# Kernel optimization log

Measured on AMD Instinct MI355X. Metric: run time of the kernel, lower is better.

Reference implementation:

```python
import jax, jax.numpy as jnp
import numpy as np

B, N, DS, DP, H, DH = 2, 512, 384, 128, 16, 64
MAX_SEQ = 2048
DI = H * DH  # inner attention dim = 1024
LN_EPS = 1e-5


def setup_inputs() -> dict:
    key = jax.random.key(0)
    ks = jax.random.split(key, 10)
    s = 0.02  # param init scale
    return {
        "single_repr": jax.random.normal(ks[0], (B, N, DS), jnp.float32),
        "pairwise_repr": jax.random.normal(ks[1], (B, N, N, DP), jnp.float32),
        "ln_gamma": jnp.ones((DP,), jnp.float32),
        "ln_beta": jnp.zeros((DP,), jnp.float32),
        "w_bias": jax.random.normal(ks[2], (DP, H), jnp.float32) * s,
        "attn_bias_bias": jax.random.normal(ks[3], (MAX_SEQ, MAX_SEQ), jnp.float32) * s,
        "w_q": jax.random.normal(ks[4], (DS, DI), jnp.float32) * s,
        "w_k": jax.random.normal(ks[5], (DS, DI), jnp.float32) * s,
        "w_v": jax.random.normal(ks[6], (DS, DI), jnp.float32) * s,
        "w_g": jax.random.normal(ks[7], (DS, DI), jnp.float32) * s,
        "w_o": jax.random.normal(ks[8], (DI, DS), jnp.float32) * s,
    }


def reference(single_repr, pairwise_repr, ln_gamma, ln_beta, w_bias,
              attn_bias_bias, w_q, w_k, w_v, w_g, w_o):
    b, n, _ = single_repr.shape
    # LayerNorm over pairwise feature dim, then project to per-head bias
    mu = pairwise_repr.mean(-1, keepdims=True)
    var = pairwise_repr.var(-1, keepdims=True)
    pr = (pairwise_repr - mu) * jax.lax.rsqrt(var + LN_EPS) * ln_gamma + ln_beta
    # ... i j h -> ... h i j, plus learned positional bias slice
    attn_bias = jnp.einsum('bijd,dh->bhij', pr, w_bias) + attn_bias_bias[:n, :n]

    # multi-head attention with additive per-head bias and sigmoid gating
    q = (single_repr @ w_q).reshape(b, n, H, DH).transpose(0, 2, 1, 3)  # bhnd
    k = (single_repr @ w_k).reshape(b, n, H, DH).transpose(0, 2, 1, 3)
    v = (single_repr @ w_v).reshape(b, n, H, DH).transpose(0, 2, 1, 3)
    scale = DH ** -0.5
    scores = jnp.einsum('bhid,bhjd->bhij', q, k) * scale + attn_bias
    attn = jax.nn.softmax(scores, axis=-1)
    o = jnp.einsum('bhij,bhjd->bhid', attn, v)
    o = o.transpose(0, 2, 1, 3).reshape(b, n, DI)
    gates = jax.nn.sigmoid(single_repr @ w_g)
    return (o * gates) @ w_o
```

## Files before the change

kernel.cpp:

```cpp
#include <hip/hip_runtime.h>
#include <hip/hip_bf16.h>

#define B_ 2
#define N_ 512
#define DS_ 384
#define DP_ 128
#define H_ 16
#define DH_ 64
#define DI_ 1024
#define MAXSEQ 2048
#define PAD 8

typedef float f32x4 __attribute__((ext_vector_type(4)));
typedef short bf16x8 __attribute__((ext_vector_type(8)));

__device__ __forceinline__ unsigned short f2b(float f) {
    unsigned int u = __builtin_bit_cast(unsigned int, f);
    u += 0x7FFFu + ((u >> 16) & 1u);
    return (unsigned short)(u >> 16);
}
__device__ __forceinline__ float b2f(unsigned short s) {
    unsigned int u = ((unsigned int)s) << 16;
    return __builtin_bit_cast(float, u);
}

__global__ __launch_bounds__(256) void k_transpose_all(const float* __restrict__ wq,
                                                       const float* __restrict__ wk,
                                                       const float* __restrict__ wv,
                                                       const float* __restrict__ wg,
                                                       const float* __restrict__ wo,
                                                       const float* __restrict__ gamma,
                                                       const float* __restrict__ beta,
                                                       const float* __restrict__ wb,
                                                       unsigned short* __restrict__ Wt,
                                                       unsigned short* __restrict__ Wot,
                                                       unsigned short* __restrict__ GhG,
                                                       float* __restrict__ SsG,
                                                       float* __restrict__ TsG) {
    int z = blockIdx.z;
    if (z == 5) {
        if (blockIdx.x || blockIdx.y) return;
        int t = threadIdx.x;
        for (int idx = t; idx < DP_ * H_; idx += 256) {
            int d = idx >> 4, h = idx & 15;
            GhG[h * DP_ + d] = f2b(gamma[d] * wb[idx]);
        }
        if (t < 32) {
            int h = t & 15;
            const float* src = (t >= 16) ? beta : gamma;
            float s = 0.f;
            for (int d = 0; d < DP_; ++d) s = fmaf(src[d], wb[d * H_ + h], s);
            if (t >= 16) TsG[h] = s; else SsG[h] = s;
        }
        return;
    }
    __shared__ float tile[32][33];
    const float* in;
    unsigned short* out;
    int R, C;
    if (z < 4) {
        in = (z == 0) ? wq : (z == 1) ? wk : (z == 2) ? wv : wg;
        out = Wt + (long)z * 1024 * 384;
        R = 384; C = 1024;
    } else {
        in = wo; out = Wot; R = 1024; C = 384;
    }
    int c0 = blockIdx.x * 32, r0 = blockIdx.y * 32;
    if (c0 >= C || r0 >= R) return;
    int tx = threadIdx.x & 31, ty = threadIdx.x >> 5;
    #pragma unroll
    for (int i = ty; i < 32; i += 8)
        tile[i][tx] = in[(long)(r0 + i) * C + (c0 + tx)];
    __syncthreads();
    #pragma unroll
    for (int i = ty; i < 32; i += 8)
        out[(long)(c0 + i) * R + (r0 + tx)] = f2b(tile[tx][i]);
}

__global__ __launch_bounds__(256) void k_bias(const float* __restrict__ pw,
                                              const float* __restrict__ abb,
                                              const unsigned short* __restrict__ GhG,
                                              const float* __restrict__ SsG,
                                              const float* __restrict__ TsG,
                                              unsigned short* __restrict__ biasP) {
    __shared__ float Xs[64 * 128];
    __shared__ float rsum[4][16] __attribute__((aligned(16)));
    __shared__ float rsq[4][16] __attribute__((aligned(16)));
    int t = threadIdx.x;
    int w = t >> 6, lane = t & 63;
    int lane15 = lane & 15, kg = lane >> 4;
    long p0 = (long)blockIdx.x * 64;
    int i_blk = (int)((p0 >> 9) & (N_ - 1));
    int j0 = (int)(p0 & (N_ - 1));
    long bb = p0 >> 18;

    const char* src = (const char*)(pw + (p0 << 7));
    char* lds = (char*)Xs;
    #pragma unroll
    for (int c = 0; c < 8; ++c) {
        int L = c * 4096 + t * 16;
        int row = L >> 9, b = L & 511;
        uint4 v = *(const uint4*)(src + L);
        *(uint4*)(lds + (row << 9) + (b ^ ((row & 7) << 4))) = v;
    }

    bf16x8 gb[4];
    #pragma unroll
    for (int kk = 0; kk < 4; ++kk)
        gb[kk] = *(const bf16x8*)&GhG[lane15 * DP_ + kk * 32 + kg * 8];
    float sh = SsG[lane15], th = TsG[lane15];
    __syncthreads();

    int row = w * 16 + lane15;
    const char* rbase = lds + (row << 9);
    int sw = (lane15 & 7) << 4;
    f32x4 xa[4], xb4[4];
    #pragma unroll
    for (int kk = 0; kk < 4; ++kk) {
        int b0 = kk * 128 + kg * 32;
        xa[kk]  = *(const f32x4*)(rbase + ((b0) ^ sw));
        xb4[kk] = *(const f32x4*)(rbase + ((b0 + 16) ^ sw));
    }
    float s = 0.f, q = 0.f;
    #pragma unroll
    for (int kk = 0; kk < 4; ++kk) {
        s += xa[kk][0] + xa[kk][1] + xa[kk][2] + xa[kk][3];
        s += xb4[kk][0] + xb4[kk][1] + xb4[kk][2] + xb4[kk][3];
        #pragma unroll
        for (int e = 0; e < 4; ++e) {
            q = fmaf(xa[kk][e], xa[kk][e], q);
            q = fmaf(xb4[kk][e], xb4[kk][e], q);
        }
    }
    s += __shfl_xor(s, 16); s += __shfl_xor(s, 32);
    q += __shfl_xor(q, 16); q += __shfl_xor(q, 32);
    if (lane < 16) { rsum[w][lane15] = s; rsq[w][lane15] = q; }

    f32x4 acc = {};
    #pragma unroll
    for (int kk = 0; kk < 4; ++kk) {
        bf16x8 a;
        unsigned short* ap = (unsigned short*)&a;
        ap[0] = f2b(xa[kk][0]);  ap[1] = f2b(xa[kk][1]);
        ap[2] = f2b(xa[kk][2]);  ap[3] = f2b(xa[kk][3]);
        ap[4] = f2b(xb4[kk][0]); ap[5] = f2b(xb4[kk][1]);
        ap[6] = f2b(xb4[kk][2]); ap[7] = f2b(xb4[kk][3]);
        acc = __builtin_amdgcn_mfma_f32_16x16x32_bf16(a, gb[kk], acc, 0, 0, 0);
    }
    int jr = w * 16 + kg * 4;
    float4 rs = *(const float4*)&rsum[w][kg * 4];
    float4 rq = *(const float4*)&rsq[w][kg * 4];
    float4 av = *(const float4*)(abb + (long)i_blk * MAXSEQ + j0 + jr);
    unsigned short* planeBase = biasP + ((bb * H_ + lane15) * N_ + i_blk) * N_ + j0;
    ushort4 res;
    float mu, var;
    mu = rs.x * (1.f / DP_); var = fmaf(rq.x, 1.f / DP_, -mu * mu);
    res.x = f2b(fmaf(rsqrtf(var + 1e-5f), acc[0] - mu * sh, th + av.x));
    mu = rs.y * (1.f / DP_); var = fmaf(rq.y, 1.f / DP_, -mu * mu);
    res.y = f2b(fmaf(rsqrtf(var + 1e-5f), acc[1] - mu * sh, th + av.y));
    mu = rs.z * (1.f / DP_); var = fmaf(rq.z, 1.f / DP_, -mu * mu);
    res.z = f2b(fmaf(rsqrtf(var + 1e-5f), acc[2] - mu * sh, th + av.z));
    mu = rs.w * (1.f / DP_); var = fmaf(rq.w, 1.f / DP_, -mu * mu);
    res.w = f2b(fmaf(rsqrtf(var + 1e-5f), acc[3] - mu * sh, th + av.w));
    *(ushort4*)(planeBase + jr) = res;
}

__global__ __launch_bounds__(256) void k_proj(const float* __restrict__ X,
                                              const unsigned short* __restrict__ Wt,
                                              unsigned short* __restrict__ Qb,
                                              unsigned short* __restrict__ Kb,
                                              unsigned short* __restrict__ Vt,
                                              unsigned short* __restrict__ Xg) {
    __shared__ unsigned short As[128][64 + PAD];
    __shared__ unsigned short Bs[128][64 + PAD];
    int m0 = blockIdx.x * 128;
    int n0 = blockIdx.y * 128;
    int t = threadIdx.x;
    int wave = t >> 6, lane = t & 63;
    int wr = wave >> 1, wc = wave & 1;
    int lane15 = lane & 15, kg = lane >> 4;
    f32x4 acc[4][4] = {};
    for (int k0 = 0; k0 < DS_; k0 += 64) {
        __syncthreads();
        {
            int r = t >> 1, half = t & 1;
            const float4* src = (const float4*)(X + (long)(m0 + r) * DS_ + k0 + half * 32);
            unsigned short* dst = &As[r][half * 32];
            #pragma unroll
            for (int ii = 0; ii < 8; ++ii) {
                float4 v = src[ii];
                dst[ii * 4 + 0] = f2b(v.x); dst[ii * 4 + 1] = f2b(v.y);
                dst[ii * 4 + 2] = f2b(v.z); dst[ii * 4 + 3] = f2b(v.w);
            }
            const uint4* wsrc = (const uint4*)(Wt + (long)(n0 + r) * DS_ + k0 + half * 32);
            uint4* wdst = (uint4*)&Bs[r][half * 32];
            wdst[0] = wsrc[0]; wdst[1] = wsrc[1]; wdst[2] = wsrc[2]; wdst[3] = wsrc[3];
        }
        __syncthreads();
        #pragma unroll
        for (int ks = 0; ks < 2; ++ks) {
            bf16x8 a[4], bb[4];
            #pragma unroll
            for (int mf = 0; mf < 4; ++mf)
                a[mf] = *(const bf16x8*)&As[wr * 64 + mf * 16 + lane15][ks * 32 + kg * 8];
            #pragma unroll
            for (int nf = 0; nf < 4; ++nf)
                bb[nf] = *(const bf16x8*)&Bs[wc * 64 + nf * 16 + lane15][ks * 32 + kg * 8];
            #pragma unroll
            for (int mf = 0; mf < 4; ++mf)
                #pragma unroll
                for (int nf = 0; nf < 4; ++nf)
                    acc[mf][nf] = __builtin_amdgcn_mfma_f32_16x16x32_bf16(a[mf], bb[nf], acc[mf][nf], 0, 0, 0);
        }
    }
    int p = n0 >> 10;
    int lgrp = lane >> 4;
    #pragma unroll
    for (int mf = 0; mf < 4; ++mf) {
        #pragma unroll
        for (int nf = 0; nf < 4; ++nf) {
            int col = n0 + wc * 64 + nf * 16 + lane15;
            int ch = col & 1023;
            int h = ch >> 6, dh = ch & 63;
            int row0 = m0 + wr * 64 + mf * 16 + lgrp * 4;
            if (p == 0 || p == 1) {
                unsigned short* base = (p == 0) ? Qb : Kb;
                float scl = (p == 0) ? 0.125f : 1.0f;
                #pragma unroll
                for (int rr = 0; rr < 4; ++rr) {
                    int rowx = row0 + rr;
                    int b = rowx >> 9, n = rowx & 511;
                    base[(((long)(b * 16 + h)) * 512 + n) * 64 + dh] = f2b(acc[mf][nf][rr] * scl);
                }
            } else if (p == 2) {
                int b = row0 >> 9, n = row0 & 511;
                ushort4 v;
                v.x = f2b(acc[mf][nf][0]); v.y = f2b(acc[mf][nf][1]);
                v.z = f2b(acc[mf][nf][2]); v.w = f2b(acc[mf][nf][3]);
                *(ushort4*)&Vt[(((long)(b * 16 + h)) * 64 + dh) * 512 + n] = v;
            } else {
                #pragma unroll
                for (int rr = 0; rr < 4; ++rr) {
                    int rowx = row0 + rr;
                    Xg[(long)rowx * 1024 + ch] = f2b(acc[mf][nf][rr]);
                }
            }
        }
    }
}

__global__ __launch_bounds__(512) void k_flash(const unsigned short* __restrict__ Qb,
                                               const unsigned short* __restrict__ Kb,
                                               const unsigned short* __restrict__ Vt,
                                               const unsigned short* __restrict__ biasP,
                                               const unsigned short* __restrict__ Xg,
                                               unsigned short* __restrict__ Og) {
    __shared__ unsigned short Kt[2][64][72];
    __shared__ unsigned short Vs[2][64][72];
    __shared__ unsigned short Bt[2][64][72];
    __shared__ unsigned short Ps[8][16][72];
    __shared__ float Mscr[4][16], Lscr[4][16];
    __shared__ float Oscr[4][16][64];
    int bh = blockIdx.y;
    int b = bh >> 4, h = bh & 15;
    int i0 = blockIdx.x * 64;
    int t = threadIdx.x, w = t >> 6, lane = t & 63;
    int g = w & 3, jg = w >> 2;
    int lane15 = lane & 15, lgrp = lane >> 4;
    int tl = t & 255;
    int rs_ = tl >> 3, cs_ = tl & 7;

    bf16x8 qf[2];
    #pragma unroll
    for (int kk = 0; kk < 2; ++kk)
        qf[kk] = *(const bf16x8*)&Qb[((long)bh * 512 + i0 + g * 16 + lane15) * 64 + kk * 32 + lgrp * 8];

    float m_run = -1e30f, l_run = 0.f;
    f32x4 o[4] = {};

    for (int jtl = 0; jtl < 4; ++jtl) {
        int j0 = (jg * 4 + jtl) * 64;
        __syncthreads();
        {
            *(uint4*)&Kt[jg][rs_][cs_ * 8] = *(const uint4*)&Kb[((long)bh * 512 + j0 + rs_) * 64 + cs_ * 8];
            *(uint4*)&Vs[jg][rs_][cs_ * 8] = *(const uint4*)&Vt[((long)bh * 64 + rs_) * 512 + j0 + cs_ * 8];
            *(uint4*)&Bt[jg][rs_][cs_ * 8] = *(const uint4*)&biasP[((long)bh * 512 + i0 + rs_) * 512 + j0 + cs_ * 8];
            int r2 = rs_ + 32;
            *(uint4*)&Kt[jg][r2][cs_ * 8] = *(const uint4*)&Kb[((long)bh * 512 + j0 + r2) * 64 + cs_ * 8];
            *(uint4*)&Vs[jg][r2][cs_ * 8] = *(const uint4*)&Vt[((long)bh * 64 + r2) * 512 + j0 + cs_ * 8];
            *(uint4*)&Bt[jg][r2][cs_ * 8] = *(const uint4*)&biasP[((long)bh * 512 + i0 + r2) * 512 + j0 + cs_ * 8];
        }
        __syncthreads();

        f32x4 s[4];
        #pragma unroll
        for (int nf = 0; nf < 4; ++nf) {
            f32x4 z = {};
            #pragma unroll
            for (int kk = 0; kk < 2; ++kk) {
                bf16x8 af = *(const bf16x8*)&Kt[jg][nf * 16 + lane15][kk * 32 + lgrp * 8];
                z = __builtin_amdgcn_mfma_f32_16x16x32_bf16(af, qf[kk], z, 0, 0, 0);
            }
            s[nf] = z;
        }
        #pragma unroll
        for (int nf = 0; nf < 4; ++nf) {
            ushort4 bv = *(const ushort4*)&Bt[jg][g * 16 + lane15][nf * 16 + lgrp * 4];
            s[nf][0] += b2f(bv.x); s[nf][1] += b2f(bv.y);
            s[nf][2] += b2f(bv.z); s[nf][3] += b2f(bv.w);
        }

        float pmax = s[0][0];
        #pragma unroll
        for (int nf = 0; nf < 4; ++nf)
            #pragma unroll
            for (int rr = 0; rr < 4; ++rr) pmax = fmaxf(pmax, s[nf][rr]);
        pmax = fmaxf(pmax, __shfl_xor(pmax, 16));
        pmax = fmaxf(pmax, __shfl_xor(pmax, 32));
        float m_new = fmaxf(m_run, pmax);
        float scale = __expf(m_run - m_new);
        float psum = 0.f;
        #pragma unroll
        for (int nf = 0; nf < 4; ++nf)
            #pragma unroll
            for (int rr = 0; rr < 4; ++rr) {
                s[nf][rr] = __expf(s[nf][rr] - m_new);
                psum += s[nf][rr];
            }
        psum += __shfl_xor(psum, 16);
        psum += __shfl_xor(psum, 32);
        l_run = l_run * scale + psum;
        m_run = m_new;
        #pragma unroll
        for (int rr = 0; rr < 4; ++rr) {
            float sc = __shfl(scale, lgrp * 4 + rr);
            #pragma unroll
            for (int nf = 0; nf < 4; ++nf) o[nf][rr] *= sc;
        }
        #pragma unroll
        for (int nf = 0; nf < 4; ++nf) {
            ushort4 pv_;
            pv_.x = f2b(s[nf][0]); pv_.y = f2b(s[nf][1]);
            pv_.z = f2b(s[nf][2]); pv_.w = f2b(s[nf][3]);
            *(ushort4*)&Ps[w][lane15][nf * 16 + lgrp * 4] = pv_;
        }
        #pragma unroll
        for (int kk = 0; kk < 2; ++kk) {
            bf16x8 pa = *(const bf16x8*)&Ps[w][lane15][kk * 32 + lgrp * 8];
            #pragma unroll
            for (int nf = 0; nf < 4; ++nf) {
                bf16x8 vb = *(const bf16x8*)&Vs[jg][nf * 16 + lane15][kk * 32 + lgrp * 8];
                o[nf] = __builtin_amdgcn_mfma_f32_16x16x32_bf16(pa, vb, o[nf], 0, 0, 0);
            }
        }
    }

    __syncthreads();
    if (jg == 1) {
        if (lane < 16) { Mscr[g][lane] = m_run; Lscr[g][lane] = l_run; }
        #pragma unroll
        for (int nf = 0; nf < 4; ++nf)
            #pragma unroll
            for (int rr = 0; rr < 4; ++rr)
                Oscr[g][lgrp * 4 + rr][nf * 16 + lane15] = o[nf][rr];
    }
    __syncthreads();
    if (jg == 0) {
        #pragma unroll
        for (int rr = 0; rr < 4; ++rr) {
            int row = lgrp * 4 + rr;
            float m1 = __shfl(m_run, row);
            float l1 = __shfl(l_run, row);
            float m2 = Mscr[g][row];
            float l2 = Lscr[g][row];
            float mm = fmaxf(m1, m2);
            float e1 = __expf(m1 - mm), e2 = __expf(m2 - mm);
            float inv = 1.f / (l1 * e1 + l2 * e2);
            long grow = (long)b * 512 + i0 + g * 16 + row;
            #pragma unroll
            for (int nf = 0; nf < 4; ++nf) {
                int dh = nf * 16 + lane15;
                float o2 = Oscr[g][row][dh];
                float val = (o[nf][rr] * e1 + o2 * e2) * inv;
                float xgv = b2f(Xg[grow * 1024 + h * 64 + dh]);
                float gate = 1.f / (1.f + __expf(-xgv));
                Og[grow * 1024 + h * 64 + dh] = f2b(val * gate);
            }
        }
    }
}

__global__ __launch_bounds__(256) void k_out(const unsigned short* __restrict__ Og,
                                             const unsigned short* __restrict__ Wot,
                                             float* __restrict__ out) {
    __shared__ unsigned short As[64][64 + PAD];
    __shared__ unsigned short Bs[64][64 + PAD];
    int m0 = blockIdx.x * 64, n0 = blockIdx.y * 64;
    int t = threadIdx.x, wave = t >> 6, lane = t & 63;
    int wr = wave >> 1, wc = wave & 1;
    int lane15 = lane & 15, kg = lane >> 4;
    f32x4 acc[2][2] = {};
    for (int k0 = 0; k0 < 1024; k0 += 64) {
        __syncthreads();
        {
            int r = t >> 2, qd = t & 3;
            const uint4* s1 = (const uint4*)(Og + (long)(m0 + r) * 1024 + k0 + qd * 16);
            uint4* d1 = (uint4*)&As[r][qd * 16];
            d1[0] = s1[0]; d1[1] = s1[1];
            const uint4* s2 = (const uint4*)(Wot + (long)(n0 + r) * 1024 + k0 + qd * 16);
            uint4* d2 = (uint4*)&Bs[r][qd * 16];
            d2[0] = s2[0]; d2[1] = s2[1];
        }
        __syncthreads();
        #pragma unroll
        for (int ks = 0; ks < 2; ++ks) {
            bf16x8 a[2], bb[2];
            #pragma unroll
            for (int mf = 0; mf < 2; ++mf)
                a[mf] = *(const bf16x8*)&As[wr * 32 + mf * 16 + lane15][ks * 32 + kg * 8];
            #pragma unroll
            for (int nf = 0; nf < 2; ++nf)
                bb[nf] = *(const bf16x8*)&Bs[wc * 32 + nf * 16 + lane15][ks * 32 + kg * 8];
            #pragma unroll
            for (int mf = 0; mf < 2; ++mf)
                #pragma unroll
                for (int nf = 0; nf < 2; ++nf)
                    acc[mf][nf] = __builtin_amdgcn_mfma_f32_16x16x32_bf16(a[mf], bb[nf], acc[mf][nf], 0, 0, 0);
        }
    }
    int lgrp = lane >> 4;
    #pragma unroll
    for (int mf = 0; mf < 2; ++mf) {
        #pragma unroll
        for (int nf = 0; nf < 2; ++nf) {
            int col = n0 + wc * 32 + nf * 16 + lane15;
            int row0 = m0 + wr * 32 + mf * 16 + lgrp * 4;
            #pragma unroll
            for (int rr = 0; rr < 4; ++rr)
                out[(long)(row0 + rr) * DS_ + col] = acc[mf][nf][rr];
        }
    }
}

extern "C" void kernel_launch(void* const* d_in, const int* in_sizes, int n_in,
                              void* d_out, int out_size, void* d_ws, size_t ws_size,
                              hipStream_t stream) {
    const float* single = (const float*)d_in[0];
    const float* pw     = (const float*)d_in[1];
    const float* gamma  = (const float*)d_in[2];
    const float* beta   = (const float*)d_in[3];
    const float* wb     = (const float*)d_in[4];
    const float* abb    = (const float*)d_in[5];
    const float* wq     = (const float*)d_in[6];
    const float* wk     = (const float*)d_in[7];
    const float* wv     = (const float*)d_in[8];
    const float* wg     = (const float*)d_in[9];
    const float* wo     = (const float*)d_in[10];
    float* out = (float*)d_out;
    char* ws = (char*)d_ws;

    unsigned short* SP  = (unsigned short*)(ws);
    unsigned short* Qb  = (unsigned short*)(ws + 16777216);
    unsigned short* Kb  = (unsigned short*)(ws + 18874368);
    unsigned short* Vt  = (unsigned short*)(ws + 20971520);
    unsigned short* Xg  = (unsigned short*)(ws + 23068672);
    unsigned short* Og  = (unsigned short*)(ws + 25165824);
    unsigned short* Wt  = (unsigned short*)(ws + 27262976);
    unsigned short* Wot = (unsigned short*)(ws + 30408704);
    unsigned short* GhG = (unsigned short*)(ws + 31195136);
    float* SsG          = (float*)(ws + 31199232);
    float* TsG          = (float*)(ws + 31199296);

    k_transpose_all<<<dim3(32, 32, 6), 256, 0, stream>>>(wq, wk, wv, wg, wo,
                                                         gamma, beta, wb,
                                                         Wt, Wot, GhG, SsG, TsG);
    k_bias<<<8192, 256, 0, stream>>>(pw, abb, GhG, SsG, TsG, SP);
    k_proj<<<dim3(8, 32), 256, 0, stream>>>(single, Wt, Qb, Kb, Vt, Xg);
    k_flash<<<dim3(8, 32), 512, 0, stream>>>(Qb, Kb, Vt, SP, Xg, Og);
    k_out<<<dim3(16, 6), 256, 0, stream>>>(Og, Wot, out);
}
```

Before: 120.8 us.

## Fuse weight transpose into bias kernel, shrink proj tiles, swizzle flash LDS

Merges the weight-transpose/bf16-convert kernel into the LayerNorm bias kernel as extra blocks. Each bias block now recomputes the gamma*w_bias fragments and the per-head sums itself, which removes a launch and the dependency on a tiny single-block prologue. The projection GEMM M-tile drops from 128 to 64 rows, doubling its grid for better occupancy. The flash kernel replaces padded LDS tiles with XOR-swizzled ones and aliases the P and O scratch buffers to cut LDS use. In exchange, the transpose blocks get scheduled alongside the heavy bias blocks, and every bias block does redundant small global loads.

Result: no change. 121.5 us (+0.6%).

```diff
diff --git a/kernel.cpp b/kernel.cpp
--- a/kernel.cpp
+++ b/kernel.cpp
@@ -24,72 +24,55 @@
     return __builtin_bit_cast(float, u);
 }
 
-__global__ __launch_bounds__(256) void k_transpose_all(const float* __restrict__ wq,
-                                                       const float* __restrict__ wk,
-                                                       const float* __restrict__ wv,
-                                                       const float* __restrict__ wg,
-                                                       const float* __restrict__ wo,
-                                                       const float* __restrict__ gamma,
-                                                       const float* __restrict__ beta,
-                                                       const float* __restrict__ wb,
-                                                       unsigned short* __restrict__ Wt,
-                                                       unsigned short* __restrict__ Wot,
-                                                       unsigned short* __restrict__ GhG,
-                                                       float* __restrict__ SsG,
-                                                       float* __restrict__ TsG) {
-    int z = blockIdx.z;
-    if (z == 5) {
-        if (blockIdx.x || blockIdx.y) return;
-        int t = threadIdx.x;
-        for (int idx = t; idx < DP_ * H_; idx += 256) {
-            int d = idx >> 4, h = idx & 15;
-            GhG[h * DP_ + d] = f2b(gamma[d] * wb[idx]);
-        }
-        if (t < 32) {
-            int h = t & 15;
-            const float* src = (t >= 16) ? beta : gamma;
-            float s = 0.f;
-            for (int d = 0; d < DP_; ++d) s = fmaf(src[d], wb[d * H_ + h], s);
-            if (t >= 16) TsG[h] = s; else SsG[h] = s;
-        }
-        return;
-    }
-    __shared__ float tile[32][33];
-    const float* in;
-    unsigned short* out;
-    int R, C;
-    if (z < 4) {
-        in = (z == 0) ? wq : (z == 1) ? wk : (z == 2) ? wv : wg;
-        out = Wt + (long)z * 1024 * 384;
-        R = 384; C = 1024;
-    } else {
-        in = wo; out = Wot; R = 1024; C = 384;
-    }
-    int c0 = blockIdx.x * 32, r0 = blockIdx.y * 32;
-    if (c0 >= C || r0 >= R) return;
-    int tx = threadIdx.x & 31, ty = threadIdx.x >> 5;
-    #pragma unroll
-    for (int i = ty; i < 32; i += 8)
-        tile[i][tx] = in[(long)(r0 + i) * C + (c0 + tx)];
-    __syncthreads();
-    #pragma unroll
-    for (int i = ty; i < 32; i += 8)
-        out[(long)(c0 + i) * R + (r0 + tx)] = f2b(tile[tx][i]);
-}
-
-__global__ __launch_bounds__(256) void k_bias(const float* __restrict__ pw,
-                                              const float* __restrict__ abb,
-                                              const unsigned short* __restrict__ GhG,
-                                              const float* __restrict__ SsG,
-                                              const float* __restrict__ TsG,
-                                              unsigned short* __restrict__ biasP) {
+#define SW(row, bc) ((bc) ^ (((row) & 7) << 4))
+
+__global__ __launch_bounds__(256) void k_pre(const float* __restrict__ pw,
+                                             const float* __restrict__ abb,
+                                             const float* __restrict__ gamma,
+                                             const float* __restrict__ beta,
+                                             const float* __restrict__ wb,
+                                             const float* __restrict__ wq,
+                                             const float* __restrict__ wk,
+                                             const float* __restrict__ wv,
+                                             const float* __restrict__ wg,
+                                             const float* __restrict__ wo,
+                                             unsigned short* __restrict__ Wt,
+                                             unsigned short* __restrict__ Wot,
+                                             unsigned short* __restrict__ biasP) {
     __shared__ float Xs[64 * 128];
     __shared__ float rsum[4][16] __attribute__((aligned(16)));
     __shared__ float rsq[4][16] __attribute__((aligned(16)));
+    int bid = blockIdx.x;
     int t = threadIdx.x;
+
+    if (bid >= 8192) {
+        int tid = bid - 8192;
+        int z = tid / 384, r = tid % 384;
+        const float* in; unsigned short* out; int C, Rr, c0, r0;
+        if (z < 4) {
+            in = (z == 0) ? wq : (z == 1) ? wk : (z == 2) ? wv : wg;
+            out = Wt + (long)z * 1024 * 384;
+            C = 1024; Rr = 384;
+            c0 = (r & 31) * 32; r0 = (r >> 5) * 32;
+        } else {
+            in = wo; out = Wot; C = 384; Rr = 1024;
+            c0 = (r % 12) * 32; r0 = (r / 12) * 32;
+        }
+        float (*tile)[33] = (float(*)[33])Xs;
+        int tx = t & 31, ty = t >> 5;
+        #pragma unroll
+        for (int i = ty; i < 32; i += 8)
+            tile[i][tx] = in[(long)(r0 + i) * C + (c0 + tx)];
+        __syncthreads();
+        #pragma unroll
+        for (int i = ty; i < 32; i += 8)
+            out[(long)(c0 + i) * Rr + (r0 + tx)] = f2b(tile[tx][i]);
+        return;
+    }
+
     int w = t >> 6, lane = t & 63;
     int lane15 = lane & 15, kg = lane >> 4;
-    long p0 = (long)blockIdx.x * 64;
+    long p0 = (long)bid * 64;
     int i_blk = (int)((p0 >> 9) & (N_ - 1));
     int j0 = (int)(p0 & (N_ - 1));
     long bb = p0 >> 18;
@@ -104,11 +87,26 @@
         *(uint4*)(lds + (row << 9) + (b ^ ((row & 7) << 4))) = v;
     }
 
+    float shp = 0.f, thp = 0.f;
     bf16x8 gb[4];
     #pragma unroll
-    for (int kk = 0; kk < 4; ++kk)
-        gb[kk] = *(const bf16x8*)&GhG[lane15 * DP_ + kk * 32 + kg * 8];
-    float sh = SsG[lane15], th = TsG[lane15];
+    for (int kk = 0; kk < 4; ++kk) {
+        bf16x8 a;
+        unsigned short* ap = (unsigned short*)&a;
+        #pragma unroll
+        for (int e = 0; e < 8; ++e) {
+            int d = kk * 32 + kg * 8 + e;
+            float wv_ = wb[d * 16 + lane15];
+            float gv = gamma[d];
+            ap[e] = f2b(gv * wv_);
+            shp = fmaf(gv, wv_, shp);
+            thp = fmaf(beta[d], wv_, thp);
+        }
+        gb[kk] = a;
+    }
+    shp += __shfl_xor(shp, 16); shp += __shfl_xor(shp, 32);
+    thp += __shfl_xor(thp, 16); thp += __shfl_xor(thp, 32);
+    float sh = shp, th = thp;
     __syncthreads();
 
     int row = w * 16 + lane15;
@@ -171,58 +169,59 @@
                                               unsigned short* __restrict__ Kb,
                                               unsigned short* __restrict__ Vt,
                                               unsigned short* __restrict__ Xg) {
-    __shared__ unsigned short As[128][64 + PAD];
+    __shared__ unsigned short As[64][64 + PAD];
     __shared__ unsigned short Bs[128][64 + PAD];
-    int m0 = blockIdx.x * 128;
+    int m0 = blockIdx.x * 64;
     int n0 = blockIdx.y * 128;
     int t = threadIdx.x;
     int wave = t >> 6, lane = t & 63;
     int wr = wave >> 1, wc = wave & 1;
     int lane15 = lane & 15, kg = lane >> 4;
-    f32x4 acc[4][4] = {};
+    int rA = t >> 2, qA = t & 3;
+    int rB = t >> 1, hB = t & 1;
+    f32x4 acc[2][4] = {};
     for (int k0 = 0; k0 < DS_; k0 += 64) {
         __syncthreads();
         {
-            int r = t >> 1, half = t & 1;
-            const float4* src = (const float4*)(X + (long)(m0 + r) * DS_ + k0 + half * 32);
-            unsigned short* dst = &As[r][half * 32];
-            #pragma unroll
-            for (int ii = 0; ii < 8; ++ii) {
-                float4 v = src[ii];
-                dst[ii * 4 + 0] = f2b(v.x); dst[ii * 4 + 1] = f2b(v.y);
-                dst[ii * 4 + 2] = f2b(v.z); dst[ii * 4 + 3] = f2b(v.w);
-            }
-            const uint4* wsrc = (const uint4*)(Wt + (long)(n0 + r) * DS_ + k0 + half * 32);
-            uint4* wdst = (uint4*)&Bs[r][half * 32];
-            wdst[0] = wsrc[0]; wdst[1] = wsrc[1]; wdst[2] = wsrc[2]; wdst[3] = wsrc[3];
+            const float4* srcA = (const float4*)(X + (long)(m0 + rA) * DS_ + k0 + qA * 16);
+            unsigned short* dstA = &As[rA][qA * 16];
+            #pragma unroll
+            for (int ii = 0; ii < 4; ++ii) {
+                float4 v = srcA[ii];
+                dstA[ii * 4 + 0] = f2b(v.x); dstA[ii * 4 + 1] = f2b(v.y);
+                dstA[ii * 4 + 2] = f2b(v.z); dstA[ii * 4 + 3] = f2b(v.w);
+            }
+            const uint4* srcB = (const uint4*)(Wt + (long)(n0 + rB) * DS_ + k0 + hB * 32);
+            uint4* dstB = (uint4*)&Bs[rB][hB * 32];
+            dstB[0] = srcB[0]; dstB[1] = srcB[1]; dstB[2] = srcB[2]; dstB[3] = srcB[3];
         }
         __syncthreads();
         #pragma unroll
         for (int ks = 0; ks < 2; ++ks) {
-            bf16x8 a[4], bb[4];
-            #pragma unroll
-            for (int mf = 0; mf < 4; ++mf)
-                a[mf] = *(const bf16x8*)&As[wr * 64 + mf * 16 + lane15][ks * 32 + kg * 8];
+            bf16x8 a[2], bbv[4];
+            #pragma unroll
+            for (int mf = 0; mf < 2; ++mf)
+                a[mf] = *(const bf16x8*)&As[wr * 32 + mf * 16 + lane15][ks * 32 + kg * 8];
             #pragma unroll
             for (int nf = 0; nf < 4; ++nf)
-                bb[nf] = *(const bf16x8*)&Bs[wc * 64 + nf * 16 + lane15][ks * 32 + kg * 8];
-            #pragma unroll
-            for (int mf = 0; mf < 4; ++mf)
+                bbv[nf] = *(const bf16x8*)&Bs[wc * 64 + nf * 16 + lane15][ks * 32 + kg * 8];
+            #pragma unroll
+            for (int mf = 0; mf < 2; ++mf)
                 #pragma unroll
                 for (int nf = 0; nf < 4; ++nf)
-                    acc[mf][nf] = __builtin_amdgcn_mfma_f32_16x16x32_bf16(a[mf], bb[nf], acc[mf][nf], 0, 0, 0);
+                    acc[mf][nf] = __builtin_amdgcn_mfma_f32_16x16x32_bf16(a[mf], bbv[nf], acc[mf][nf], 0, 0, 0);
         }
     }
     int p = n0 >> 10;
     int lgrp = lane >> 4;
     #pragma unroll
-    for (int mf = 0; mf < 4; ++mf) {
+    for (int mf = 0; mf < 2; ++mf) {
         #pragma unroll
         for (int nf = 0; nf < 4; ++nf) {
             int col = n0 + wc * 64 + nf * 16 + lane15;
             int ch = col & 1023;
             int h = ch >> 6, dh = ch & 63;
-            int row0 = m0 + wr * 64 + mf * 16 + lgrp * 4;
+            int row0 = m0 + wr * 32 + mf * 16 + lgrp * 4;
             if (p == 0 || p == 1) {
                 unsigned short* base = (p == 0) ? Qb : Kb;
                 float scl = (p == 0) ? 0.125f : 1.0f;
@@ -255,12 +254,13 @@
                                                const unsigned short* __restrict__ biasP,
                                                const unsigned short* __restrict__ Xg,
                                                unsigned short* __restrict__ Og) {
-    __shared__ unsigned short Kt[2][64][72];
-    __shared__ unsigned short Vs[2][64][72];
-    __shared__ unsigned short Bt[2][64][72];
-    __shared__ unsigned short Ps[8][16][72];
+    __shared__ unsigned short Kt[2][64][64];
+    __shared__ unsigned short Vs[2][64][64];
+    __shared__ unsigned short Bt[2][64][64];
+    __shared__ char PsOscr[16384];
     __shared__ float Mscr[4][16], Lscr[4][16];
-    __shared__ float Oscr[4][16][64];
+    unsigned short (*Ps)[16][64] = (unsigned short(*)[16][64])PsOscr;
+    float (*Oscr)[16][64] = (float(*)[16][64])PsOscr;
     int bh = blockIdx.y;
     int b = bh >> 4, h = bh & 15;
     int i0 = blockIdx.x * 64;
@@ -282,13 +282,19 @@
         int j0 = (jg * 4 + jtl) * 64;
         __syncthreads();
         {
-            *(uint4*)&Kt[jg][rs_][cs_ * 8] = *(const uint4*)&Kb[((long)bh * 512 + j0 + rs_) * 64 + cs_ * 8];
-            *(uint4*)&Vs[jg][rs_][cs_ * 8] = *(const uint4*)&Vt[((long)bh * 64 + rs_) * 512 + j0 + cs_ * 8];
-            *(uint4*)&Bt[jg][rs_][cs_ * 8] = *(const uint4*)&biasP[((long)bh * 512 + i0 + rs_) * 512 + j0 + cs_ * 8];
             int r2 = rs_ + 32;
-            *(uint4*)&Kt[jg][r2][cs_ * 8] = *(const uint4*)&Kb[((long)bh * 512 + j0 + r2) * 64 + cs_ * 8];
-            *(uint4*)&Vs[jg][r2][cs_ * 8] = *(const uint4*)&Vt[((long)bh * 64 + r2) * 512 + j0 + cs_ * 8];
-            *(uint4*)&Bt[jg][r2][cs_ * 8] = *(const uint4*)&biasP[((long)bh * 512 + i0 + r2) * 512 + j0 + cs_ * 8];
+            *(uint4*)((char*)&Kt[jg][rs_][0] + SW(rs_, cs_ * 16)) =
+                *(const uint4*)&Kb[((long)bh * 512 + j0 + rs_) * 64 + cs_ * 8];
+            *(uint4*)((char*)&Vs[jg][rs_][0] + SW(rs_, cs_ * 16)) =
+                *(const uint4*)&Vt[((long)bh * 64 + rs_) * 512 + j0 + cs_ * 8];
+            *(uint4*)((char*)&Bt[jg][rs_][0] + SW(rs_, cs_ * 16)) =
+                *(const uint4*)&biasP[((long)bh * 512 + i0 + rs_) * 512 + j0 + cs_ * 8];
+            *(uint4*)((char*)&Kt[jg][r2][0] + SW(r2, cs_ * 16)) =
+                *(const uint4*)&Kb[((long)bh * 512 + j0 + r2) * 64 + cs_ * 8];
+            *(uint4*)((char*)&Vs[jg][r2][0] + SW(r2, cs_ * 16)) =
+                *(const uint4*)&Vt[((long)bh * 64 + r2) * 512 + j0 + cs_ * 8];
+            *(uint4*)((char*)&Bt[jg][r2][0] + SW(r2, cs_ * 16)) =
+                *(const uint4*)&biasP[((long)bh * 512 + i0 + r2) * 512 + j0 + cs_ * 8];
         }
         __syncthreads();
 
@@ -298,14 +304,16 @@
             f32x4 z = {};
             #pragma unroll
             for (int kk = 0; kk < 2; ++kk) {
-                bf16x8 af = *(const bf16x8*)&Kt[jg][nf * 16 + lane15][kk * 32 + lgrp * 8];
+                bf16x8 af = *(const bf16x8*)((const char*)&Kt[jg][nf * 16 + lane15][0] +
+                                             SW(lane15, kk * 64 + lgrp * 16));
                 z = __builtin_amdgcn_mfma_f32_16x16x32_bf16(af, qf[kk], z, 0, 0, 0);
             }
             s[nf] = z;
         }
         #pragma unroll
         for (int nf = 0; nf < 4; ++nf) {
-            ushort4 bv = *(const ushort4*)&Bt[jg][g * 16 + lane15][nf * 16 + lgrp * 4];
+            ushort4 bv = *(const ushort4*)((const char*)&Bt[jg][g * 16 + lane15][0] +
+                                           SW(lane15, nf * 32 + lgrp * 8));
             s[nf][0] += b2f(bv.x); s[nf][1] += b2f(bv.y);
             s[nf][2] += b2f(bv.z); s[nf][3] += b2f(bv.w);
         }
@@ -342,14 +350,16 @@
             ushort4 pv_;
             pv_.x = f2b(s[nf][0]); pv_.y = f2b(s[nf][1]);
             pv_.z = f2b(s[nf][2]); pv_.w = f2b(s[nf][3]);
-            *(ushort4*)&Ps[w][lane15][nf * 16 + lgrp * 4] = pv_;
+            *(ushort4*)((char*)&Ps[w][lane15][0] + SW(lane15, nf * 32 + lgrp * 8)) = pv_;
         }
         #pragma unroll
         for (int kk = 0; kk < 2; ++kk) {
-            bf16x8 pa = *(const bf16x8*)&Ps[w][lane15][kk * 32 + lgrp * 8];
+            bf16x8 pa = *(const bf16x8*)((const char*)&Ps[w][lane15][0] +
+                                         SW(lane15, kk * 64 + lgrp * 16));
             #pragma unroll
             for (int nf = 0; nf < 4; ++nf) {
-                bf16x8 vb = *(const bf16x8*)&Vs[jg][nf * 16 + lane15][kk * 32 + lgrp * 8];
+                bf16x8 vb = *(const bf16x8*)((const char*)&Vs[jg][nf * 16 + lane15][0] +
+                                             SW(lane15, kk * 64 + lgrp * 16));
                 o[nf] = __builtin_amdgcn_mfma_f32_16x16x32_bf16(pa, vb, o[nf], 0, 0, 0);
             }
         }
@@ -414,18 +424,18 @@
         __syncthreads();
         #pragma unroll
         for (int ks = 0; ks < 2; ++ks) {
-            bf16x8 a[2], bb[2];
+            bf16x8 a[2], bbv[2];
             #pragma unroll
             for (int mf = 0; mf < 2; ++mf)
                 a[mf] = *(const bf16x8*)&As[wr * 32 + mf * 16 + lane15][ks * 32 + kg * 8];
             #pragma unroll
             for (int nf = 0; nf < 2; ++nf)
-                bb[nf] = *(const bf16x8*)&Bs[wc * 32 + nf * 16 + lane15][ks * 32 + kg * 8];
+                bbv[nf] = *(const bf16x8*)&Bs[wc * 32 + nf * 16 + lane15][ks * 32 + kg * 8];
             #pragma unroll
             for (int mf = 0; mf < 2; ++mf)
                 #pragma unroll
                 for (int nf = 0; nf < 2; ++nf)
-                    acc[mf][nf] = __builtin_amdgcn_mfma_f32_16x16x32_bf16(a[mf], bb[nf], acc[mf][nf], 0, 0, 0);
+                    acc[mf][nf] = __builtin_amdgcn_mfma_f32_16x16x32_bf16(a[mf], bbv[nf], acc[mf][nf], 0, 0, 0);
         }
     }
     int lgrp = lane >> 4;
@@ -467,15 +477,10 @@
     unsigned short* Og  = (unsigned short*)(ws + 25165824);
     unsigned short* Wt  = (unsigned short*)(ws + 27262976);
     unsigned short* Wot = (unsigned short*)(ws + 30408704);
-    unsigned short* GhG = (unsigned short*)(ws + 31195136);
-    float* SsG          = (float*)(ws + 31199232);
-    float* TsG          = (float*)(ws + 31199296);
-
-    k_transpose_all<<<dim3(32, 32, 6), 256, 0, stream>>>(wq, wk, wv, wg, wo,
-                                                         gamma, beta, wb,
-                                                         Wt, Wot, GhG, SsG, TsG);
-    k_bias<<<8192, 256, 0, stream>>>(pw, abb, GhG, SsG, TsG, SP);
-    k_proj<<<dim3(8, 32), 256, 0, stream>>>(single, Wt, Qb, Kb, Vt, Xg);
+
+    k_pre<<<10112, 256, 0, stream>>>(pw, abb, gamma, beta, wb,
+                                     wq, wk, wv, wg, wo, Wt, Wot, SP);
+    k_proj<<<dim3(16, 32), 256, 0, stream>>>(single, Wt, Qb, Kb, Vt, Xg);
     k_flash<<<dim3(8, 32), 512, 0, stream>>>(Qb, Kb, Vt, SP, Xg, Og);
     k_out<<<dim3(16, 6), 256, 0, stream>>>(Og, Wot, out);
 }
```
